# Kernel tuning notes

Hardware: AMD Instinct MI355X
Metric: run time of the kernel (lower is better)

## Reference

```python
import jax, jax.numpy as jnp
import numpy as np

B, N_IN, N_OPS, E = 2048, 64, 1024, 64   # graphs, leaf inputs, operations, embed_size
N_OIO, N_TIO, VOCAB = 4, 4, 1000         # one-input ops, two-input ops, embedding rows


def setup_inputs() -> dict:
    key = jax.random.key(0)
    ks = jax.random.split(key, 8)
    rng = np.random.default_rng(0)
    # random valid DAG topology: op j may read any node with index < N_IN + j
    op_kind = rng.integers(0, 2, N_OPS)
    t_oio = rng.integers(0, N_OIO, N_OPS)
    t_tio = rng.integers(0, N_TIO, N_OPS)
    op_w_idx = np.where(op_kind == 0, t_oio, N_OIO + t_tio).astype(np.int32)
    op_in1 = np.array([rng.integers(0, N_IN + j) for j in range(N_OPS)], dtype=np.int32)
    op_in2 = np.array([rng.integers(0, N_IN + j) for j in range(N_OPS)], dtype=np.int32)
    s = 0.1  # keep relu chain numerically tame
    return {
        "input_ids": jax.random.randint(ks[0], (B, N_IN), 0, VOCAB, dtype=jnp.int32),
        "op_w_idx": jnp.asarray(op_w_idx),
        "op_in1": jnp.asarray(op_in1),
        "op_in2": jnp.asarray(op_in2),
        "embedding": jax.random.normal(ks[1], (VOCAB, E), jnp.float32) * s,
        "oio_W": jax.random.normal(ks[2], (N_OIO, E, E), jnp.float32) * s,
        "oio_b": jax.random.normal(ks[3], (N_OIO, E), jnp.float32) * s,
        "tio_W": jax.random.normal(ks[4], (N_TIO, 2 * E, E), jnp.float32) * s,
        "tio_b": jax.random.normal(ks[5], (N_TIO, E), jnp.float32) * s,
        "final_W": jax.random.normal(ks[6], (E, 1), jnp.float32) * s,
        "final_b": jax.random.normal(ks[7], (1,), jnp.float32) * s,
    }


def reference(input_ids, op_w_idx, op_in1, op_in2, embedding,
              oio_W, oio_b, tio_W, tio_b, final_W, final_b):
    # Unify weights: one-input Linear(E,E) padded with zeros on the x2 half,
    # so cat(x1, x2) @ W_pad + b == x1 @ W + b (identical math to the torch module).
    W_all = jnp.concatenate(
        [jnp.concatenate([oio_W, jnp.zeros_like(oio_W)], axis=1), tio_W], axis=0)  # (8, 2E, E)
    b_all = jnp.concatenate([oio_b, tio_b], axis=0)                                # (8, E)

    leaves = embedding[input_ids]                                   # (B, N_IN, E)
    nodes0 = jnp.concatenate(
        [leaves, jnp.zeros((B, N_OPS, E), leaves.dtype)], axis=1)   # (B, N_IN+N_OPS, E)

    def step(nodes, op):
        j, widx, i1, i2 = op
        x1 = jnp.take(nodes, i1, axis=1)                            # (B, E)
        x2 = jnp.take(nodes, i2, axis=1)                            # (B, E)
        h = jax.nn.relu(jnp.concatenate([x1, x2], axis=-1) @ W_all[widx] + b_all[widx])
        nodes = jax.lax.dynamic_update_slice(nodes, h[:, None, :], (0, N_IN + j, 0))
        return nodes, None

    xs = (jnp.arange(N_OPS, dtype=jnp.int32), op_w_idx, op_in1, op_in2)
    nodes, _ = jax.lax.scan(step, nodes0, xs)

    # operation_counter: final Linear(E, 1) on the last produced node tensor
    return nodes[:, -1, :] @ final_W + final_b                      # (B, 1)
```

## Files before the change

kernel.cpp:

```cpp
#include <hip/hip_runtime.h>

#define NIN 64
#define NOPS 1024
#define NB 2048
#define NNODES 1088
#define SLAB_SH 18

#define WS_SCHED 0u
#define WS_LEV   8192u
#define WS_WT    16384u
#define WS_BIAS  147456u
#define WS_NODES 163840u

#define LM_LINES 0u
#define LM_SCHED 65536u
#define LM_MSTA  73728u
#define LM_TOTAL 77824u

typedef unsigned int u32;
typedef unsigned short u16;
typedef unsigned long long u64;
typedef _Float16 f16;
typedef _Float16 f16x8 __attribute__((ext_vector_type(8)));
typedef _Float16 f16x4 __attribute__((ext_vector_type(4)));
typedef float f32x4 __attribute__((ext_vector_type(4)));

#define MFMA16(a, b, c) __builtin_amdgcn_mfma_f32_16x16x32_f16((a), (b), (c), 0, 0, 0)


__global__ __launch_bounds__(1024) void k_sched(const int* __restrict__ wxv,
                                                const int* __restrict__ in1v,
                                                const int* __restrict__ in2v,
                                                char* __restrict__ ws, int cap) {
  __shared__ int s1[NOPS], s2[NOPS], sw[NOPS], slv[NOPS];
  __shared__ int lcnt[132];
  __shared__ int cnt2[1032];
  __shared__ u64 s_pack[NOPS];
  __shared__ int dl[NNODES], slot_of[NNODES];
  __shared__ int stk[2304];
  __shared__ int opPos[NOPS];
  __shared__ unsigned char needG[NOPS];
  __shared__ int s_flags[3];
  __shared__ int s_nlev, s_top, s_err;
  const int j = threadIdx.x;
  s1[j] = in1v[j]; s2[j] = in2v[j]; sw[j] = wxv[j]; slv[j] = 1;
  needG[j] = 0;
  if (j < 132) lcnt[j] = 0;
  if (j < 1032) cnt2[j] = 0;
  if (j < 3) s_flags[j] = 0;
  if (j == 0) { s_nlev = 0; s_err = 0; }
  __syncthreads();
  for (int it = 0; it < NOPS + 1; ++it) {
    int c = it % 3;
    int p1 = s1[j];
    int l1 = (p1 >= NIN) ? slv[p1 - NIN] : 0;
    int l2 = 0;
    if (sw[j] >= 4) { int p2 = s2[j]; l2 = (p2 >= NIN) ? slv[p2 - NIN] : 0; }
    int nl = 1 + (l1 > l2 ? l1 : l2);
    if (nl != slv[j]) { slv[j] = nl; s_flags[c] = 1; }
    if (j == 0) s_flags[(it + 1) % 3] = 0;
    __syncthreads();
    if (!s_flags[c]) break;
  }
  atomicMax(&s_nlev, slv[j]);
  __syncthreads();
  u32* wl = (u32*)(ws + WS_LEV);
  const int nlev = s_nlev;
  if (nlev > 127) { if (j == 0) { wl[0] = 0; wl[1] = 0; wl[2] = 1; } return; }
  atomicAdd(&lcnt[slv[j]], 1);
  atomicAdd(&cnt2[slv[j] * 8 + sw[j]], 1);
  __syncthreads();
  if (j == 0) {
    int acc = 0;
    for (int L = 1; L <= nlev; ++L) { int c = lcnt[L]; lcnt[L] = acc; acc += c; }
  }
  __syncthreads();
  int base = -1;
  if (j >= 8 && j < (nlev + 1) * 8) {
    int L = j >> 3, mm = j & 7;
    int s = lcnt[L];
    for (int q = 0; q < mm; ++q) s += cnt2[L * 8 + q];
    base = s;
  }
  u16* msta = (u16*)(ws + WS_LEV + 4096);
  for (int t = j; t < 2048; t += 1024) msta[t] = (u16)NOPS;
  __syncthreads();
  if (base >= 0) { cnt2[j] = base; msta[j] = (u16)base; }
  __syncthreads();
  { int slot = atomicAdd(&cnt2[slv[j] * 8 + sw[j]], 1);
    u64 p = (u64)(u32)s1[j] | ((u64)(u32)s2[j] << 11) | ((u64)(u32)sw[j] << 22) | ((u64)(u32)j << 25);
    s_pack[slot] = p;
    opPos[j] = slot - lcnt[slv[j]]; }
  __syncthreads();
  if (j == NOPS - 1) needG[j] = 1;
  { int L = slv[j];
    int i1n = s1[j];
    if (i1n >= NIN) { int p = i1n - NIN; if (!(slv[p] == L - 1 && opPos[p] < 64)) needG[p] = 1; }
    if (sw[j] >= 4) {
      int i2n = s2[j];
      if (i2n >= NIN) { int p = i2n - NIN; if (!(slv[p] == L - 1 && opPos[p] < 64)) needG[p] = 1; }
    } }
  for (int t = j; t < NNODES; t += 1024) dl[t] = (t < NIN) ? 0 : slv[t - NIN];
  __syncthreads();
  atomicMax(&dl[s1[j]], slv[j]);
  if (sw[j] >= 4) atomicMax(&dl[s2[j]], slv[j]);
  __syncthreads();
  if (j == 0) dl[NNODES - 1] = nlev + 1;
  if (j < NIN) slot_of[j] = j;
  { int S = cap - 64; if (S > 1152) S = 1152;
    for (int t = j; t < S; t += 1024) stk[t] = 64 + t;
    if (j == 0) s_top = S; }
  __syncthreads();
  for (int L = 1; L <= nlev; ++L) {
    for (int t = j; t < NNODES; t += 1024)
      if (dl[t] == L - 1) {
        int p = atomicAdd(&s_top, 1);
        if (p >= 0 && p < 2304) stk[p] = slot_of[t];
      }
    __syncthreads();
    if (slv[j] == L) {
      int p = atomicSub(&s_top, 1);
      int s;
      if (p >= 1) s = stk[p - 1]; else { s = 64; s_err = 1; }
      slot_of[NIN + j] = s;
    }
    __syncthreads();
  }
  {
    u64 m = s_pack[j];
    int i1n = (int)(m & 2047u), i2n = (int)((m >> 11) & 2047u);
    u32 wxn = (u32)((m >> 22) & 7u);
    int opn = (int)((m >> 25) & 2047u);
    int Lop = slv[opn];
    int two = (wxn >= 4);
    if (!two) i2n = i1n;
    u32 f1 = 0, p1 = 0, f2 = 0, p2 = 0;
    if (i1n >= NIN) { int p = i1n - NIN;
      if (slv[p] == Lop - 1 && opPos[p] < 64) { f1 = 1; p1 = (u32)opPos[p]; } }
    if (i2n >= NIN) { int p = i2n - NIN;
      if (slv[p] == Lop - 1 && opPos[p] < 64) { f2 = 1; p2 = (u32)opPos[p]; } }
    u32 op_pos = (u32)opPos[opn];
    u32 ldsout = (op_pos < 64) ? 1u : 0u;
    u32 gout   = needG[opn] ? 1u : 0u;
    u32 s1slot = (u32)slot_of[i1n];
    u32 s2slot = (u32)slot_of[i2n];
    u64 nm = (u64)s1slot | ((u64)s2slot << 11) | ((u64)wxn << 22)
           | ((u64)(u32)slot_of[NIN + opn] << 25)
           | ((u64)p1 << 36) | ((u64)f1 << 43)
           | ((u64)p2 << 44) | ((u64)f2 << 51)
           | ((u64)(op_pos & 63u) << 52) | ((u64)ldsout << 59)
           | ((u64)gout << 60);
    ((u64*)(ws + WS_SCHED))[j] = nm;
  }
  if (j == 0) {
    wl[0] = (u32)nlev;
    wl[1] = (u32)slot_of[NNODES - 1];
    wl[2] = s_err ? 1u : 0u;
  }
}

__global__ __launch_bounds__(256) void k_prep(const int* __restrict__ ids,
                                              const float* __restrict__ emb,
                                              const float* __restrict__ oW,
                                              const float* __restrict__ ob,
                                              const float* __restrict__ tW,
                                              const float* __restrict__ tb,
                                              char* __restrict__ ws) {
  int p = blockIdx.x * 256 + threadIdx.x;
  int i = p >> 11, b = p & 2047;
  int id = ids[b * 64 + i];
  const f32x4* src = (const f32x4*)(emb + (u32)id * 64u);
  f16x8* dst = (f16x8*)(ws + WS_NODES + ((u32)i << SLAB_SH) + (u32)b * 128u);
  #pragma unroll
  for (int q = 0; q < 8; ++q) {
    f32x4 lo = src[2 * q], hi = src[2 * q + 1];
    f16x8 v = { (f16)lo.x, (f16)lo.y, (f16)lo.z, (f16)lo.w,
                (f16)hi.x, (f16)hi.y, (f16)hi.z, (f16)hi.w };
    dst[q] = v;
  }
  if (blockIdx.x < 64) {
    f16* wt = (f16*)(ws + WS_WT);
    int t = blockIdx.x * 256 + threadIdx.x;
    #pragma unroll
    for (int q = 0; q < 4; ++q) {
      int e = t * 4 + q;
      int mat = e >> 13, n = (e >> 7) & 63, k = e & 127;
      float v;
      if (mat < 4) v = (k < 64) ? oW[mat * 4096 + k * 64 + n] : 0.f;
      else         v = tW[(mat - 4) * 8192 + k * 64 + n];
      wt[e] = (f16)v;
    }
    if (blockIdx.x == 0) {
      float* bs = (float*)(ws + WS_BIAS);
      for (int q = threadIdx.x; q < 512; q += 256)
        bs[q] = (q < 256) ? ob[q] : tb[q - 256];
    }
  }
}

__global__ __launch_bounds__(512, 4) void k_main(char* __restrict__ ws) {
  extern __shared__ char lds[];
  const int tid = threadIdx.x;
  const u32* wl = (const u32*)(ws + WS_LEV);
  if (wl[2]) return;
  for (int t = tid; t < NOPS; t += 512)
    ((u64*)(lds + LM_SCHED))[t] = ((const u64*)(ws + WS_SCHED))[t];
  for (int t = tid; t < 1024; t += 512)
    ((u32*)(lds + LM_MSTA))[t] = ((const u32*)(ws + WS_LEV + 4096))[t];
  const int nlev = (int)wl[0];

  const int lane   = tid & 63;
  const int m      = tid >> 6;
  const int lhi    = lane >> 4, llo = lane & 15;
  const int op_sub = llo >> 2;
  const int brow   = llo & 3;
  const int r0     = blockIdx.x * 4;
  char* nodes = ws + WS_NODES;

  const f16* wp = (const f16*)(ws + WS_WT) + m * 8192 + llo * 128 + lhi * 8;
  f16x8 W00 = *(const f16x8*)(wp +        0), W01 = *(const f16x8*)(wp +       32),
        W10 = *(const f16x8*)(wp + 2048 + 0), W11 = *(const f16x8*)(wp + 2048 + 32),
        W20 = *(const f16x8*)(wp + 4096 + 0), W21 = *(const f16x8*)(wp + 4096 + 32),
        W30 = *(const f16x8*)(wp + 6144 + 0), W31 = *(const f16x8*)(wp + 6144 + 32);
  f16x8 W02 = {}, W03 = {}, W12 = {}, W13 = {}, W22 = {}, W23 = {}, W32 = {}, W33 = {};
  if (m >= 4) {
    W02 = *(const f16x8*)(wp +        64); W03 = *(const f16x8*)(wp +        96);
    W12 = *(const f16x8*)(wp + 2048 + 64); W13 = *(const f16x8*)(wp + 2048 + 96);
    W22 = *(const f16x8*)(wp + 4096 + 64); W23 = *(const f16x8*)(wp + 4096 + 96);
    W32 = *(const f16x8*)(wp + 6144 + 64); W33 = *(const f16x8*)(wp + 6144 + 96);
  }
  asm volatile("" : "+v"(W00), "+v"(W01), "+v"(W10), "+v"(W11),
                    "+v"(W20), "+v"(W21), "+v"(W30), "+v"(W31));
  asm volatile("" : "+v"(W02), "+v"(W03), "+v"(W12), "+v"(W13),
                    "+v"(W22), "+v"(W23), "+v"(W32), "+v"(W33));
  const float* bsp = (const float*)(ws + WS_BIAS) + m * 64 + lhi * 4;
  const f32x4 B0 = *(const f32x4*)(bsp),      B1 = *(const f32x4*)(bsp + 16),
              B2 = *(const f32x4*)(bsp + 32), B3 = *(const f32x4*)(bsp + 48);
  __syncthreads();

  const u64* s_sched = (const u64*)(lds + LM_SCHED);
  const u16* s_msta  = (const u16*)(lds + LM_MSTA);

  const u32 a_off  = (u32)((r0 + brow) * 128 + lhi * 16);
  const u32 st_off = (u32)((r0 + brow) * 128 + lhi * 8);
  const u32 key  = (u32)(brow << 4);
  const u32 bA   = (u32)(brow * 128);
  const u32 cA0  = (u32)((lhi * 16)      ^ key);
  const u32 cA1  = (u32)((lhi * 16 + 64) ^ key);
  const u32 cS0  = (u32)((      lhi * 8) ^ key);
  const u32 cS1  = (u32)(( 32 + lhi * 8) ^ key);
  const u32 cS2  = (u32)(( 64 + lhi * 8) ^ key);
  const u32 cS3  = (u32)(( 96 + lhi * 8) ^ key);

  for (int L = 1; L <= nlev; ++L) {
    const u32 rb = (u32)(((L - 1) & 1) << 15);
    const u32 wb = (u32)((L & 1) << 15);
    int k0 = (int)s_msta[L * 8 + m];
    int k1 = (int)s_msta[L * 8 + m + 1];
    k0 = __builtin_amdgcn_readfirstlane(k0);
    k1 = __builtin_amdgcn_readfirstlane(k1);
    const int ke = k1 - 1;
    for (int g = k0; g < k1; g += 4) {
      int kop = g + op_sub; kop = kop > ke ? ke : kop;
      u64 md = s_sched[kop];
      f16x8 a0, a1;
      if ((md >> 43) & 1) {
        u32 pos = (u32)(md >> 36) & 63u;
        const char* l1 = lds + rb + (pos << 9);
        u32 px = (pos & 3u) << 5;
        a0 = *(const f16x8*)(l1 + bA + (cA0 ^ px));
        a1 = *(const f16x8*)(l1 + bA + (cA1 ^ px));
      } else {
        const char* b1 = nodes + ((u64)((u32)md & 2047u) << SLAB_SH) + a_off;
        a0 = *(const f16x8*)(b1);
        a1 = *(const f16x8*)(b1 + 64);
      }
      f16x8 a2 = {}, a3 = {};
      if (m >= 4) {
        if ((md >> 51) & 1) {
          u32 pos = (u32)(md >> 44) & 63u;
          const char* l2 = lds + rb + (pos << 9);
          u32 px = (pos & 3u) << 5;
          a2 = *(const f16x8*)(l2 + bA + (cA0 ^ px));
          a3 = *(const f16x8*)(l2 + bA + (cA1 ^ px));
        } else {
          const char* b2 = nodes + ((u64)(((u32)(md >> 11)) & 2047u) << SLAB_SH) + a_off;
          a2 = *(const f16x8*)(b2);
          a3 = *(const f16x8*)(b2 + 64);
        }
      }
      f32x4 c0 = B0, c1 = B1, c2 = B2, c3 = B3;
      __builtin_amdgcn_s_setprio(1);
      c0 = MFMA16(W00, a0, c0); c0 = MFMA16(W01, a1, c0);
      c1 = MFMA16(W10, a0, c1); c1 = MFMA16(W11, a1, c1);
      c2 = MFMA16(W20, a0, c2); c2 = MFMA16(W21, a1, c2);
      c3 = MFMA16(W30, a0, c3); c3 = MFMA16(W31, a1, c3);
      if (m >= 4) {
        c0 = MFMA16(W02, a2, c0); c0 = MFMA16(W03, a3, c0);
        c1 = MFMA16(W12, a2, c1); c1 = MFMA16(W13, a3, c1);
        c2 = MFMA16(W22, a2, c2); c2 = MFMA16(W23, a3, c2);
        c3 = MFMA16(W32, a2, c3); c3 = MFMA16(W33, a3, c3);
      }
      __builtin_amdgcn_s_setprio(0);
      f16x4 r0v = { (f16)(c0.x > 0.f ? c0.x : 0.f), (f16)(c0.y > 0.f ? c0.y : 0.f),
                    (f16)(c0.z > 0.f ? c0.z : 0.f), (f16)(c0.w > 0.f ? c0.w : 0.f) };
      f16x4 r1v = { (f16)(c1.x > 0.f ? c1.x : 0.f), (f16)(c1.y > 0.f ? c1.y : 0.f),
                    (f16)(c1.z > 0.f ? c1.z : 0.f), (f16)(c1.w > 0.f ? c1.w : 0.f) };
      f16x4 r2v = { (f16)(c2.x > 0.f ? c2.x : 0.f), (f16)(c2.y > 0.f ? c2.y : 0.f),
                    (f16)(c2.z > 0.f ? c2.z : 0.f), (f16)(c2.w > 0.f ? c2.w : 0.f) };
      f16x4 r3v = { (f16)(c3.x > 0.f ? c3.x : 0.f), (f16)(c3.y > 0.f ? c3.y : 0.f),
                    (f16)(c3.z > 0.f ? c3.z : 0.f), (f16)(c3.w > 0.f ? c3.w : 0.f) };
      if ((md >> 59) & 1) {
        u32 opos = (u32)(md >> 52) & 63u;
        char* lp = lds + wb + (opos << 9);
        u32 px = (opos & 3u) << 5;
        *(f16x4*)(lp + bA + (cS0 ^ px)) = r0v;
        *(f16x4*)(lp + bA + (cS1 ^ px)) = r1v;
        *(f16x4*)(lp + bA + (cS2 ^ px)) = r2v;
        *(f16x4*)(lp + bA + (cS3 ^ px)) = r3v;
      }
      if ((md >> 60) & 1) {
        char* st = nodes + (((u64)((md >> 25) & 2047u)) << SLAB_SH) + st_off;
        *(f16x4*)(st)      = r0v;
        *(f16x4*)(st + 32) = r1v;
        *(f16x4*)(st + 64) = r2v;
        *(f16x4*)(st + 96) = r3v;
      }
    }
    __syncthreads();
  }
}

__global__ __launch_bounds__(256) void k_final(const float* __restrict__ fw,
                                               const float* __restrict__ fb,
                                               const char* __restrict__ ws,
                                               float* __restrict__ out) {
  __shared__ float s_fw[64];
  int t = threadIdx.x;
  if (t < 64) s_fw[t] = fw[t];
  __syncthreads();
  int b = blockIdx.x * 256 + t;
  const u32* wl = (const u32*)(ws + WS_LEV);
  if (wl[2]) { out[b] = 0.f; return; }
  u32 slot = wl[1];
  const f16x8* last = (const f16x8*)(ws + WS_NODES + ((u64)slot << SLAB_SH) + (u32)b * 128u);
  float acc = fb[0];
  #pragma unroll
  for (int q = 0; q < 8; ++q) {
    f16x8 v = last[q];
    #pragma unroll
    for (int e = 0; e < 8; ++e) acc += (float)v[e] * s_fw[q * 8 + e];
  }
  out[b] = acc;
}

extern "C" void kernel_launch(void* const* d_in, const int* in_sizes, int n_in,
                              void* d_out, int out_size, void* d_ws, size_t ws_size,
                              hipStream_t stream) {
  const int*   ids = (const int*)d_in[0];
  const int*   wx  = (const int*)d_in[1];
  const int*   i1  = (const int*)d_in[2];
  const int*   i2  = (const int*)d_in[3];
  const float* emb = (const float*)d_in[4];
  const float* oW  = (const float*)d_in[5];
  const float* ob  = (const float*)d_in[6];
  const float* tW  = (const float*)d_in[7];
  const float* tb  = (const float*)d_in[8];
  const float* fw  = (const float*)d_in[9];
  const float* fb  = (const float*)d_in[10];
  char* ws = (char*)d_ws;
  float* out = (float*)d_out;

  int cap = (int)((ws_size > (size_t)WS_NODES) ? ((ws_size - WS_NODES) >> SLAB_SH) : 0);
  if (cap < 80) return;
  if (cap > 2047) cap = 2047;

  hipLaunchKernelGGL(k_sched, dim3(1),   dim3(1024), 0, stream, wx, i1, i2, ws, cap);
  hipLaunchKernelGGL(k_prep,  dim3(512), dim3(256),  0, stream, ids, emb, oW, ob, tW, tb, ws);
  hipLaunchKernelGGL(k_main,  dim3(512), dim3(512),  LM_TOTAL, stream, ws);
  hipLaunchKernelGGL(k_final, dim3(8),   dim3(256),  0, stream, fw, fb, ws, out);
}
```

Measured before the change: 120.7 us.

## Cap levels at four ops per matrix, fuse prep into scheduler and final into main

```diff
diff --git a/kernel.cpp b/kernel.cpp
--- a/kernel.cpp
+++ b/kernel.cpp
@@ -13,9 +13,9 @@
 #define WS_NODES 163840u
 
 #define LM_LINES 0u
-#define LM_SCHED 65536u
-#define LM_MSTA  73728u
-#define LM_TOTAL 77824u
+#define LM_SCHED 32768u
+#define LM_MSTA  40960u
+#define LM_TOTAL 45056u
 
 typedef unsigned int u32;
 typedef unsigned short u16;
@@ -28,47 +28,96 @@
 #define MFMA16(a, b, c) __builtin_amdgcn_mfma_f32_16x16x32_f16((a), (b), (c), 0, 0, 0)
 
 
-__global__ __launch_bounds__(1024) void k_sched(const int* __restrict__ wxv,
-                                                const int* __restrict__ in1v,
-                                                const int* __restrict__ in2v,
-                                                char* __restrict__ ws, int cap) {
-  __shared__ int s1[NOPS], s2[NOPS], sw[NOPS], slv[NOPS];
+__global__ __launch_bounds__(1024) void k_sp(const int* __restrict__ ids,
+                                             const float* __restrict__ emb,
+                                             const float* __restrict__ oW,
+                                             const float* __restrict__ ob,
+                                             const float* __restrict__ tW,
+                                             const float* __restrict__ tb,
+                                             const int* __restrict__ wxv,
+                                             const int* __restrict__ in1v,
+                                             const int* __restrict__ in2v,
+                                             char* __restrict__ ws, int cap) {
+  __shared__ int s1[NOPS], s2[NOPS], sw[NOPS], lvl[NOPS], posA[NOPS];
   __shared__ int lcnt[132];
   __shared__ int cnt2[1032];
   __shared__ u64 s_pack[NOPS];
   __shared__ int dl[NNODES], slot_of[NNODES];
   __shared__ int stk[2304];
-  __shared__ int opPos[NOPS];
   __shared__ unsigned char needG[NOPS];
-  __shared__ int s_flags[3];
-  __shared__ int s_nlev, s_top, s_err;
-  const int j = threadIdx.x;
-  s1[j] = in1v[j]; s2[j] = in2v[j]; sw[j] = wxv[j]; slv[j] = 1;
-  needG[j] = 0;
+  __shared__ int ccnt[8];
+  __shared__ int s_nlev, s_top, s_err, s_nsched;
+
+  const int tid = threadIdx.x;
+  if (blockIdx.x != 0) {
+    int bid = (int)blockIdx.x - 1;
+    if (tid < 256) {
+      int p = bid * 256 + tid;
+      int i = p >> 11, b = p & 2047;
+      int id = ids[b * 64 + i];
+      const f32x4* src = (const f32x4*)(emb + (u32)id * 64u);
+      f16x8* dst = (f16x8*)(ws + WS_NODES + ((u32)i << SLAB_SH) + (u32)b * 128u);
+      #pragma unroll
+      for (int q = 0; q < 8; ++q) {
+        f32x4 lo = src[2 * q], hi = src[2 * q + 1];
+        f16x8 v = { (f16)lo.x, (f16)lo.y, (f16)lo.z, (f16)lo.w,
+                    (f16)hi.x, (f16)hi.y, (f16)hi.z, (f16)hi.w };
+        dst[q] = v;
+      }
+    } else if (tid < 512) {
+      if (bid < 64) {
+        f16* wt = (f16*)(ws + WS_WT);
+        int t = bid * 256 + (tid - 256);
+        #pragma unroll
+        for (int q = 0; q < 4; ++q) {
+          int e = t * 4 + q;
+          int mat = e >> 13, n = (e >> 7) & 63, k = e & 127;
+          float v;
+          if (mat < 4) v = (k < 64) ? oW[mat * 4096 + k * 64 + n] : 0.f;
+          else         v = tW[(mat - 4) * 8192 + k * 64 + n];
+          wt[e] = (f16)v;
+        }
+      }
+    } else {
+      if (bid == 0) {
+        int q = tid - 512;
+        float* bs = (float*)(ws + WS_BIAS);
+        bs[q] = (q < 256) ? ob[q] : tb[q - 256];
+      }
+    }
+    return;
+  }
+
+  const int j = tid;
+  s1[j] = in1v[j]; s2[j] = in2v[j]; sw[j] = wxv[j];
+  lvl[j] = 0; posA[j] = 0; needG[j] = 0;
   if (j < 132) lcnt[j] = 0;
   if (j < 1032) cnt2[j] = 0;
-  if (j < 3) s_flags[j] = 0;
-  if (j == 0) { s_nlev = 0; s_err = 0; }
-  __syncthreads();
-  for (int it = 0; it < NOPS + 1; ++it) {
-    int c = it % 3;
-    int p1 = s1[j];
-    int l1 = (p1 >= NIN) ? slv[p1 - NIN] : 0;
-    int l2 = 0;
-    if (sw[j] >= 4) { int p2 = s2[j]; l2 = (p2 >= NIN) ? slv[p2 - NIN] : 0; }
-    int nl = 1 + (l1 > l2 ? l1 : l2);
-    if (nl != slv[j]) { slv[j] = nl; s_flags[c] = 1; }
-    if (j == 0) s_flags[(it + 1) % 3] = 0;
-    __syncthreads();
-    if (!s_flags[c]) break;
-  }
-  atomicMax(&s_nlev, slv[j]);
+  if (j == 0) { s_nlev = 0; s_err = 0; s_nsched = 0; }
   __syncthreads();
   u32* wl = (u32*)(ws + WS_LEV);
+
+  const int myp1 = s1[j], myp2 = s2[j], mym = sw[j];
+  const bool two = mym >= 4;
+  for (int L = 1; L <= 126; ++L) {
+    bool d1 = (myp1 < NIN) || (lvl[myp1 - NIN] != 0);
+    bool d2 = (!two) || (myp2 < NIN) || (lvl[myp2 - NIN] != 0);
+    bool rdy = (lvl[j] == 0) && d1 && d2;
+    if (j < 8) ccnt[j] = 0;
+    __syncthreads();
+    if (rdy) {
+      int pos = atomicAdd(&ccnt[mym], 1);
+      if (pos < 4) { lvl[j] = L; posA[j] = pos; atomicAdd(&s_nsched, 1); }
+    }
+    __syncthreads();
+    if (s_nsched == NOPS) { if (j == 0) s_nlev = L; break; }
+  }
+  __syncthreads();
   const int nlev = s_nlev;
-  if (nlev > 127) { if (j == 0) { wl[0] = 0; wl[1] = 0; wl[2] = 1; } return; }
-  atomicAdd(&lcnt[slv[j]], 1);
-  atomicAdd(&cnt2[slv[j] * 8 + sw[j]], 1);
+  if (nlev == 0) { if (j == 0) { wl[0] = 0; wl[1] = 0; wl[2] = 1; } return; }
+
+  atomicAdd(&lcnt[lvl[j]], 1);
+  atomicAdd(&cnt2[lvl[j] * 8 + mym], 1);
   __syncthreads();
   if (j == 0) {
     int acc = 0;
@@ -87,23 +136,17 @@
   __syncthreads();
   if (base >= 0) { cnt2[j] = base; msta[j] = (u16)base; }
   __syncthreads();
-  { int slot = atomicAdd(&cnt2[slv[j] * 8 + sw[j]], 1);
-    u64 p = (u64)(u32)s1[j] | ((u64)(u32)s2[j] << 11) | ((u64)(u32)sw[j] << 22) | ((u64)(u32)j << 25);
-    s_pack[slot] = p;
-    opPos[j] = slot - lcnt[slv[j]]; }
-  __syncthreads();
+  { int idx = cnt2[lvl[j] * 8 + mym] + posA[j];
+    u64 p = (u64)(u32)myp1 | ((u64)(u32)myp2 << 11) | ((u64)(u32)mym << 22) | ((u64)(u32)j << 25);
+    s_pack[idx] = p; }
   if (j == NOPS - 1) needG[j] = 1;
-  { int L = slv[j];
-    int i1n = s1[j];
-    if (i1n >= NIN) { int p = i1n - NIN; if (!(slv[p] == L - 1 && opPos[p] < 64)) needG[p] = 1; }
-    if (sw[j] >= 4) {
-      int i2n = s2[j];
-      if (i2n >= NIN) { int p = i2n - NIN; if (!(slv[p] == L - 1 && opPos[p] < 64)) needG[p] = 1; }
-    } }
-  for (int t = j; t < NNODES; t += 1024) dl[t] = (t < NIN) ? 0 : slv[t - NIN];
-  __syncthreads();
-  atomicMax(&dl[s1[j]], slv[j]);
-  if (sw[j] >= 4) atomicMax(&dl[s2[j]], slv[j]);
+  { int L = lvl[j];
+    if (myp1 >= NIN) { int p = myp1 - NIN; if (L - lvl[p] >= 2) needG[p] = 1; }
+    if (two && myp2 >= NIN) { int p = myp2 - NIN; if (L - lvl[p] >= 2) needG[p] = 1; } }
+  for (int t = j; t < NNODES; t += 1024) dl[t] = (t < NIN) ? 0 : lvl[t - NIN];
+  __syncthreads();
+  atomicMax(&dl[myp1], lvl[j]);
+  if (two) atomicMax(&dl[myp2], lvl[j]);
   __syncthreads();
   if (j == 0) dl[NNODES - 1] = nlev + 1;
   if (j < NIN) slot_of[j] = j;
@@ -118,7 +161,7 @@
         if (p >= 0 && p < 2304) stk[p] = slot_of[t];
       }
     __syncthreads();
-    if (slv[j] == L) {
+    if (lvl[j] == L) {
       int p = atomicSub(&s_top, 1);
       int s;
       if (p >= 1) s = stk[p - 1]; else { s = 64; s_err = 1; }
@@ -131,24 +174,20 @@
     int i1n = (int)(m & 2047u), i2n = (int)((m >> 11) & 2047u);
     u32 wxn = (u32)((m >> 22) & 7u);
     int opn = (int)((m >> 25) & 2047u);
-    int Lop = slv[opn];
-    int two = (wxn >= 4);
-    if (!two) i2n = i1n;
-    u32 f1 = 0, p1 = 0, f2 = 0, p2 = 0;
+    int Lop = lvl[opn];
+    if (wxn < 4) i2n = i1n;
+    u32 f1 = 0, l1 = 0, f2 = 0, l2 = 0;
     if (i1n >= NIN) { int p = i1n - NIN;
-      if (slv[p] == Lop - 1 && opPos[p] < 64) { f1 = 1; p1 = (u32)opPos[p]; } }
+      if (lvl[p] == Lop - 1) { f1 = 1; l1 = (u32)(sw[p] * 4 + posA[p]); } }
     if (i2n >= NIN) { int p = i2n - NIN;
-      if (slv[p] == Lop - 1 && opPos[p] < 64) { f2 = 1; p2 = (u32)opPos[p]; } }
-    u32 op_pos = (u32)opPos[opn];
-    u32 ldsout = (op_pos < 64) ? 1u : 0u;
-    u32 gout   = needG[opn] ? 1u : 0u;
-    u32 s1slot = (u32)slot_of[i1n];
-    u32 s2slot = (u32)slot_of[i2n];
-    u64 nm = (u64)s1slot | ((u64)s2slot << 11) | ((u64)wxn << 22)
+      if (lvl[p] == Lop - 1) { f2 = 1; l2 = (u32)(sw[p] * 4 + posA[p]); } }
+    u32 outline = (u32)(sw[opn] * 4 + posA[opn]);
+    u32 gout    = needG[opn] ? 1u : 0u;
+    u64 nm = (u64)(u32)slot_of[i1n] | ((u64)(u32)slot_of[i2n] << 11) | ((u64)wxn << 22)
            | ((u64)(u32)slot_of[NIN + opn] << 25)
-           | ((u64)p1 << 36) | ((u64)f1 << 43)
-           | ((u64)p2 << 44) | ((u64)f2 << 51)
-           | ((u64)(op_pos & 63u) << 52) | ((u64)ldsout << 59)
+           | ((u64)l1 << 36) | ((u64)f1 << 43)
+           | ((u64)l2 << 44) | ((u64)f2 << 51)
+           | ((u64)outline << 52) | (1ull << 59)
            | ((u64)gout << 60);
     ((u64*)(ws + WS_SCHED))[j] = nm;
   }
@@ -159,46 +198,10 @@
   }
 }
 
-__global__ __launch_bounds__(256) void k_prep(const int* __restrict__ ids,
-                                              const float* __restrict__ emb,
-                                              const float* __restrict__ oW,
-                                              const float* __restrict__ ob,
-                                              const float* __restrict__ tW,
-                                              const float* __restrict__ tb,
-                                              char* __restrict__ ws) {
-  int p = blockIdx.x * 256 + threadIdx.x;
-  int i = p >> 11, b = p & 2047;
-  int id = ids[b * 64 + i];
-  const f32x4* src = (const f32x4*)(emb + (u32)id * 64u);
-  f16x8* dst = (f16x8*)(ws + WS_NODES + ((u32)i << SLAB_SH) + (u32)b * 128u);
-  #pragma unroll
-  for (int q = 0; q < 8; ++q) {
-    f32x4 lo = src[2 * q], hi = src[2 * q + 1];
-    f16x8 v = { (f16)lo.x, (f16)lo.y, (f16)lo.z, (f16)lo.w,
-                (f16)hi.x, (f16)hi.y, (f16)hi.z, (f16)hi.w };
-    dst[q] = v;
-  }
-  if (blockIdx.x < 64) {
-    f16* wt = (f16*)(ws + WS_WT);
-    int t = blockIdx.x * 256 + threadIdx.x;
-    #pragma unroll
-    for (int q = 0; q < 4; ++q) {
-      int e = t * 4 + q;
-      int mat = e >> 13, n = (e >> 7) & 63, k = e & 127;
-      float v;
-      if (mat < 4) v = (k < 64) ? oW[mat * 4096 + k * 64 + n] : 0.f;
-      else         v = tW[(mat - 4) * 8192 + k * 64 + n];
-      wt[e] = (f16)v;
-    }
-    if (blockIdx.x == 0) {
-      float* bs = (float*)(ws + WS_BIAS);
-      for (int q = threadIdx.x; q < 512; q += 256)
-        bs[q] = (q < 256) ? ob[q] : tb[q - 256];
-    }
-  }
-}
-
-__global__ __launch_bounds__(512, 4) void k_main(char* __restrict__ ws) {
+__global__ __launch_bounds__(512, 4) void k_main(char* __restrict__ ws,
+                                                 const float* __restrict__ fw,
+                                                 const float* __restrict__ fb,
+                                                 float* __restrict__ out) {
   extern __shared__ char lds[];
   const int tid = threadIdx.x;
   const u32* wl = (const u32*)(ws + WS_LEV);
@@ -253,8 +256,8 @@
   const u32 cS3  = (u32)(( 96 + lhi * 8) ^ key);
 
   for (int L = 1; L <= nlev; ++L) {
-    const u32 rb = (u32)(((L - 1) & 1) << 15);
-    const u32 wb = (u32)((L & 1) << 15);
+    const u32 rb = (u32)(((L - 1) & 1) << 14);
+    const u32 wb = (u32)((L & 1) << 14);
     int k0 = (int)s_msta[L * 8 + m];
     int k1 = (int)s_msta[L * 8 + m + 1];
     k0 = __builtin_amdgcn_readfirstlane(k0);
@@ -265,9 +268,9 @@
       u64 md = s_sched[kop];
       f16x8 a0, a1;
       if ((md >> 43) & 1) {
-        u32 pos = (u32)(md >> 36) & 63u;
-        const char* l1 = lds + rb + (pos << 9);
-        u32 px = (pos & 3u) << 5;
+        u32 line = (u32)(md >> 36) & 63u;
+        const char* l1 = lds + rb + (line << 9);
+        u32 px = (line & 3u) << 5;
         a0 = *(const f16x8*)(l1 + bA + (cA0 ^ px));
         a1 = *(const f16x8*)(l1 + bA + (cA1 ^ px));
       } else {
@@ -278,9 +281,9 @@
       f16x8 a2 = {}, a3 = {};
       if (m >= 4) {
         if ((md >> 51) & 1) {
-          u32 pos = (u32)(md >> 44) & 63u;
-          const char* l2 = lds + rb + (pos << 9);
-          u32 px = (pos & 3u) << 5;
+          u32 line = (u32)(md >> 44) & 63u;
+          const char* l2 = lds + rb + (line << 9);
+          u32 px = (line & 3u) << 5;
           a2 = *(const f16x8*)(l2 + bA + (cA0 ^ px));
           a3 = *(const f16x8*)(l2 + bA + (cA1 ^ px));
         } else {
@@ -310,10 +313,10 @@
                     (f16)(c2.z > 0.f ? c2.z : 0.f), (f16)(c2.w > 0.f ? c2.w : 0.f) };
       f16x4 r3v = { (f16)(c3.x > 0.f ? c3.x : 0.f), (f16)(c3.y > 0.f ? c3.y : 0.f),
                     (f16)(c3.z > 0.f ? c3.z : 0.f), (f16)(c3.w > 0.f ? c3.w : 0.f) };
-      if ((md >> 59) & 1) {
-        u32 opos = (u32)(md >> 52) & 63u;
-        char* lp = lds + wb + (opos << 9);
-        u32 px = (opos & 3u) << 5;
+      {
+        u32 oline = (u32)(md >> 52) & 63u;
+        char* lp = lds + wb + (oline << 9);
+        u32 px = (oline & 3u) << 5;
         *(f16x4*)(lp + bA + (cS0 ^ px)) = r0v;
         *(f16x4*)(lp + bA + (cS1 ^ px)) = r1v;
         *(f16x4*)(lp + bA + (cS2 ^ px)) = r2v;
@@ -329,29 +332,22 @@
     }
     __syncthreads();
   }
-}
-
-__global__ __launch_bounds__(256) void k_final(const float* __restrict__ fw,
-                                               const float* __restrict__ fb,
-                                               const char* __restrict__ ws,
-                                               float* __restrict__ out) {
-  __shared__ float s_fw[64];
-  int t = threadIdx.x;
-  if (t < 64) s_fw[t] = fw[t];
-  __syncthreads();
-  int b = blockIdx.x * 256 + t;
-  const u32* wl = (const u32*)(ws + WS_LEV);
-  if (wl[2]) { out[b] = 0.f; return; }
-  u32 slot = wl[1];
-  const f16x8* last = (const f16x8*)(ws + WS_NODES + ((u64)slot << SLAB_SH) + (u32)b * 128u);
-  float acc = fb[0];
-  #pragma unroll
-  for (int q = 0; q < 8; ++q) {
-    f16x8 v = last[q];
-    #pragma unroll
-    for (int e = 0; e < 8; ++e) acc += (float)v[e] * s_fw[q * 8 + e];
-  }
-  out[b] = acc;
+
+  {
+    u32 slot = wl[1];
+    if (m < 4) {
+      int row = m;
+      const f16* src = (const f16*)(nodes + ((u64)slot << SLAB_SH) + (u32)(r0 + row) * 128u);
+      float v = (float)src[lane] * fw[lane];
+      v += __shfl_down(v, 32);
+      v += __shfl_down(v, 16);
+      v += __shfl_down(v, 8);
+      v += __shfl_down(v, 4);
+      v += __shfl_down(v, 2);
+      v += __shfl_down(v, 1);
+      if (lane == 0) out[r0 + row] = v + fb[0];
+    }
+  }
 }
 
 extern "C" void kernel_launch(void* const* d_in, const int* in_sizes, int n_in,
@@ -375,8 +371,7 @@
   if (cap < 80) return;
   if (cap > 2047) cap = 2047;
 
-  hipLaunchKernelGGL(k_sched, dim3(1),   dim3(1024), 0, stream, wx, i1, i2, ws, cap);
-  hipLaunchKernelGGL(k_prep,  dim3(512), dim3(256),  0, stream, ids, emb, oW, ob, tW, tb, ws);
-  hipLaunchKernelGGL(k_main,  dim3(512), dim3(512),  LM_TOTAL, stream, ws);
-  hipLaunchKernelGGL(k_final, dim3(8),   dim3(256),  0, stream, fw, fb, ws, out);
+  hipLaunchKernelGGL(k_sp,   dim3(513), dim3(1024), 0, stream,
+                     ids, emb, oW, ob, tW, tb, wx, i1, i2, ws, cap);
+  hipLaunchKernelGGL(k_main, dim3(512), dim3(512),  LM_TOTAL, stream, ws, fw, fb, out);
 }
```

Result: slower. 134.0 us (+10.9%).

## Fuse schedule and prep kernels and fold final projection into main kernel

Applied to the files above, without the earlier changes.

```diff
diff --git a/kernel.cpp b/kernel.cpp
--- a/kernel.cpp
+++ b/kernel.cpp
@@ -28,10 +28,56 @@
 #define MFMA16(a, b, c) __builtin_amdgcn_mfma_f32_16x16x32_f16((a), (b), (c), 0, 0, 0)
 
 
-__global__ __launch_bounds__(1024) void k_sched(const int* __restrict__ wxv,
-                                                const int* __restrict__ in1v,
-                                                const int* __restrict__ in2v,
-                                                char* __restrict__ ws, int cap) {
+__global__ __launch_bounds__(1024) void k_sp(const int* __restrict__ ids,
+                                             const float* __restrict__ emb,
+                                             const float* __restrict__ oW,
+                                             const float* __restrict__ ob,
+                                             const float* __restrict__ tW,
+                                             const float* __restrict__ tb,
+                                             const int* __restrict__ wxv,
+                                             const int* __restrict__ in1v,
+                                             const int* __restrict__ in2v,
+                                             char* __restrict__ ws, int cap) {
+  const int tid = threadIdx.x;
+  if (blockIdx.x != 0) {
+    int bid = (int)blockIdx.x - 1;
+    if (tid < 256) {
+      int p = bid * 256 + tid;
+      int i = p >> 11, b = p & 2047;
+      int id = ids[b * 64 + i];
+      const f32x4* src = (const f32x4*)(emb + (u32)id * 64u);
+      f16x8* dst = (f16x8*)(ws + WS_NODES + ((u32)i << SLAB_SH) + (u32)b * 128u);
+      #pragma unroll
+      for (int q = 0; q < 8; ++q) {
+        f32x4 lo = src[2 * q], hi = src[2 * q + 1];
+        f16x8 v = { (f16)lo.x, (f16)lo.y, (f16)lo.z, (f16)lo.w,
+                    (f16)hi.x, (f16)hi.y, (f16)hi.z, (f16)hi.w };
+        dst[q] = v;
+      }
+    } else if (tid < 512) {
+      if (bid < 64) {
+        f16* wt = (f16*)(ws + WS_WT);
+        int t = bid * 256 + (tid - 256);
+        #pragma unroll
+        for (int q = 0; q < 4; ++q) {
+          int e = t * 4 + q;
+          int mat = e >> 13, n = (e >> 7) & 63, k = e & 127;
+          float v;
+          if (mat < 4) v = (k < 64) ? oW[mat * 4096 + k * 64 + n] : 0.f;
+          else         v = tW[(mat - 4) * 8192 + k * 64 + n];
+          wt[e] = (f16)v;
+        }
+      }
+    } else {
+      if (bid == 0) {
+        int q = tid - 512;
+        float* bs = (float*)(ws + WS_BIAS);
+        bs[q] = (q < 256) ? ob[q] : tb[q - 256];
+      }
+    }
+    return;
+  }
+
   __shared__ int s1[NOPS], s2[NOPS], sw[NOPS], slv[NOPS];
   __shared__ int lcnt[132];
   __shared__ int cnt2[1032];
@@ -42,7 +88,7 @@
   __shared__ unsigned char needG[NOPS];
   __shared__ int s_flags[3];
   __shared__ int s_nlev, s_top, s_err;
-  const int j = threadIdx.x;
+  const int j = tid;
   s1[j] = in1v[j]; s2[j] = in2v[j]; sw[j] = wxv[j]; slv[j] = 1;
   needG[j] = 0;
   if (j < 132) lcnt[j] = 0;
@@ -159,46 +205,10 @@
   }
 }
 
-__global__ __launch_bounds__(256) void k_prep(const int* __restrict__ ids,
-                                              const float* __restrict__ emb,
-                                              const float* __restrict__ oW,
-                                              const float* __restrict__ ob,
-                                              const float* __restrict__ tW,
-                                              const float* __restrict__ tb,
-                                              char* __restrict__ ws) {
-  int p = blockIdx.x * 256 + threadIdx.x;
-  int i = p >> 11, b = p & 2047;
-  int id = ids[b * 64 + i];
-  const f32x4* src = (const f32x4*)(emb + (u32)id * 64u);
-  f16x8* dst = (f16x8*)(ws + WS_NODES + ((u32)i << SLAB_SH) + (u32)b * 128u);
-  #pragma unroll
-  for (int q = 0; q < 8; ++q) {
-    f32x4 lo = src[2 * q], hi = src[2 * q + 1];
-    f16x8 v = { (f16)lo.x, (f16)lo.y, (f16)lo.z, (f16)lo.w,
-                (f16)hi.x, (f16)hi.y, (f16)hi.z, (f16)hi.w };
-    dst[q] = v;
-  }
-  if (blockIdx.x < 64) {
-    f16* wt = (f16*)(ws + WS_WT);
-    int t = blockIdx.x * 256 + threadIdx.x;
-    #pragma unroll
-    for (int q = 0; q < 4; ++q) {
-      int e = t * 4 + q;
-      int mat = e >> 13, n = (e >> 7) & 63, k = e & 127;
-      float v;
-      if (mat < 4) v = (k < 64) ? oW[mat * 4096 + k * 64 + n] : 0.f;
-      else         v = tW[(mat - 4) * 8192 + k * 64 + n];
-      wt[e] = (f16)v;
-    }
-    if (blockIdx.x == 0) {
-      float* bs = (float*)(ws + WS_BIAS);
-      for (int q = threadIdx.x; q < 512; q += 256)
-        bs[q] = (q < 256) ? ob[q] : tb[q - 256];
-    }
-  }
-}
-
-__global__ __launch_bounds__(512, 4) void k_main(char* __restrict__ ws) {
+__global__ __launch_bounds__(512, 4) void k_main(char* __restrict__ ws,
+                                                 const float* __restrict__ fw,
+                                                 const float* __restrict__ fb,
+                                                 float* __restrict__ out) {
   extern __shared__ char lds[];
   const int tid = threadIdx.x;
   const u32* wl = (const u32*)(ws + WS_LEV);
@@ -329,29 +339,22 @@
     }
     __syncthreads();
   }
-}
-
-__global__ __launch_bounds__(256) void k_final(const float* __restrict__ fw,
-                                               const float* __restrict__ fb,
-                                               const char* __restrict__ ws,
-                                               float* __restrict__ out) {
-  __shared__ float s_fw[64];
-  int t = threadIdx.x;
-  if (t < 64) s_fw[t] = fw[t];
-  __syncthreads();
-  int b = blockIdx.x * 256 + t;
-  const u32* wl = (const u32*)(ws + WS_LEV);
-  if (wl[2]) { out[b] = 0.f; return; }
-  u32 slot = wl[1];
-  const f16x8* last = (const f16x8*)(ws + WS_NODES + ((u64)slot << SLAB_SH) + (u32)b * 128u);
-  float acc = fb[0];
-  #pragma unroll
-  for (int q = 0; q < 8; ++q) {
-    f16x8 v = last[q];
-    #pragma unroll
-    for (int e = 0; e < 8; ++e) acc += (float)v[e] * s_fw[q * 8 + e];
-  }
-  out[b] = acc;
+
+  {
+    u32 slot = wl[1];
+    if (m < 4) {
+      int row = m;
+      const f16* src = (const f16*)(nodes + ((u64)slot << SLAB_SH) + (u32)(r0 + row) * 128u);
+      float v = (float)src[lane] * fw[lane];
+      v += __shfl_down(v, 32);
+      v += __shfl_down(v, 16);
+      v += __shfl_down(v, 8);
+      v += __shfl_down(v, 4);
+      v += __shfl_down(v, 2);
+      v += __shfl_down(v, 1);
+      if (lane == 0) out[r0 + row] = v + fb[0];
+    }
+  }
 }
 
 extern "C" void kernel_launch(void* const* d_in, const int* in_sizes, int n_in,
@@ -375,8 +378,7 @@
   if (cap < 80) return;
   if (cap > 2047) cap = 2047;
 
-  hipLaunchKernelGGL(k_sched, dim3(1),   dim3(1024), 0, stream, wx, i1, i2, ws, cap);
-  hipLaunchKernelGGL(k_prep,  dim3(512), dim3(256),  0, stream, ids, emb, oW, ob, tW, tb, ws);
-  hipLaunchKernelGGL(k_main,  dim3(512), dim3(512),  LM_TOTAL, stream, ws);
-  hipLaunchKernelGGL(k_final, dim3(8),   dim3(256),  0, stream, fw, fb, ws, out);
+  hipLaunchKernelGGL(k_sp,   dim3(513), dim3(1024), 0, stream,
+                     ids, emb, oW, ob, tW, tb, wx, i1, i2, ws, cap);
+  hipLaunchKernelGGL(k_main, dim3(512), dim3(512),  LM_TOTAL, stream, ws, fw, fb, out);
 }
```

Result: faster. 106.6 us, median of 2 (-11.8%).
